# Kernel optimization log

Measured on AMD Instinct MI355X. Metric: run time of the kernel, lower is better.

Reference implementation:

```python
import jax, jax.numpy as jnp
import numpy as np

B, N, D = 64, 1024, 128
K = 6  # hardcoded neighbor count in the module


def setup_inputs() -> dict:
    key = jax.random.key(0)
    ks = jax.random.split(key, 11)
    def lin(k, out_d, in_d):
        kw, kb = jax.random.split(k)
        s = 1.0 / np.sqrt(in_d)
        W = jax.random.uniform(kw, (out_d, in_d), minval=-s, maxval=s, dtype=jnp.float32)
        b = jax.random.uniform(kb, (out_d,), minval=-s, maxval=s, dtype=jnp.float32)
        return W, b
    loc = jax.random.uniform(ks[0], (B, N, 2), dtype=jnp.float32)
    deadline = jax.random.uniform(ks[1], (B, N), dtype=jnp.float32)
    depot = jax.random.uniform(ks[2], (B, 2), dtype=jnp.float32)
    W3d, b3d = lin(ks[3], D, 3)
    W2d, b2d = lin(ks[4], D, 2)
    Wnb, bnb = lin(ks[5], D, K * D)
    Wdep, bdep = lin(ks[6], D, 2)
    return {"loc": loc, "deadline": deadline, "depot": depot,
            "W3d": W3d, "b3d": b3d, "W2d": W2d, "b2d": b2d,
            "Wnb": Wnb, "bnb": bnb, "Wdep": Wdep, "bdep": bdep}


def reference(loc, deadline, depot, W3d, b3d, W2d, b2d, Wnb, bnb, Wdep, bdep):
    x = jnp.concatenate([loc, deadline[:, :, None]], axis=2)  # [B,N,3]
    x2 = x[:, :, 0:2]                                          # [B,N,2]
    F2 = jnp.einsum('bnf,df->bnd', x2, W2d) + b2d              # [B,N,D]
    F3 = jnp.einsum('bnf,df->bnd', x, W3d) + b3d               # [B,N,D]
    # pairwise euclidean distances; indices are non-differentiable -> stop_gradient
    diff = x2[:, None, :, :] - x2[:, :, None, :]               # [B,N,N,2]
    dist = jnp.sqrt(jnp.sum(diff * diff, axis=-1))             # [B,N,N]
    _, neighbors = jax.lax.top_k(jax.lax.stop_gradient(-dist), K)  # [B,N,K] smallest dists (incl. self)
    # faithful quirk: original does F0_embedding_2d[:, neighbors][0] == gather from batch-0 embeddings
    nb = F2[0][neighbors]                                      # [B,N,K,D]
    nb_c = nb.reshape(nb.shape[0], nb.shape[1], K * nb.shape[3])  # [B,N,K*D]
    Fn = jnp.einsum('bnf,df->bnd', nb_c, Wnb) + bnb            # [B,N,D]
    Ff = Fn + F3
    dep = depot @ Wdep.T + bdep                                 # [B,D]
    h = jax.nn.leaky_relu(jnp.concatenate([dep[:, None, :], Ff], axis=1), negative_slope=0.01)
    return h, h.mean(axis=1)
```

## Files before the change

kernel.cpp:

```cpp
#include <hip/hip_runtime.h>
#include <hip/hip_bf16.h>

#define CB 64
#define CN 1024
#define CD 128
#define CK 6

typedef __attribute__((ext_vector_type(8))) short short8;
typedef __attribute__((ext_vector_type(4))) float floatx4;

__device__ __forceinline__ unsigned short f2bf(float f) {
    union { float f; unsigned u; } c; c.f = f;
    unsigned u = c.u;
    u += 0x7FFFu + ((u >> 16) & 1u);
    return (unsigned short)(u >> 16);
}

#define WS_G      0
#define WS_NBRS   3145728
#define WS_IDS    3932160
#define WS_STARTS 4063232
#define WS_PART   4129024

struct SortSM { float2 pts[CN]; int cnt[256]; int base[256]; };
struct GSM    { unsigned short As[128 * 40]; unsigned short Bs[128 * 40]; };
union GridSM  { SortSM s; GSM g; };

__global__ void __launch_bounds__(256) k_gridg(
    const float* __restrict__ loc,
    const float* __restrict__ W2d,
    const float* __restrict__ b2d,
    const float* __restrict__ Wnb,
    unsigned short* __restrict__ ids,
    int* __restrict__ starts,
    float* __restrict__ G)
{
    __shared__ GridSM sm;
    int t = threadIdx.x;

    if (blockIdx.x < 64) {
        int b = blockIdx.x;
        const float2* lb = (const float2*)loc + b * CN;
#pragma unroll
        for (int r = 0; r < 4; ++r) sm.s.pts[t + r * 256] = lb[t + r * 256];
        sm.s.cnt[t] = 0;
        __syncthreads();
        int mycell[4];
#pragma unroll
        for (int r = 0; r < 4; ++r) {
            float2 p = sm.s.pts[t * 4 + r];
            int cx = (int)(p.x * 16.0f); cx = cx > 15 ? 15 : cx;
            int cy = (int)(p.y * 16.0f); cy = cy > 15 ? 15 : cy;
            mycell[r] = (cy << 4) + cx;
            atomicAdd(&sm.s.cnt[mycell[r]], 1);
        }
        __syncthreads();
        for (int off = 1; off < 256; off <<= 1) {
            int u = (t >= off) ? sm.s.cnt[t - off] : 0;
            __syncthreads();
            sm.s.cnt[t] += u;
            __syncthreads();
        }
        int excl = (t == 0) ? 0 : sm.s.cnt[t - 1];
        sm.s.base[t] = excl;
        starts[b * 257 + t] = excl;
        if (t == 255) starts[b * 257 + 256] = sm.s.cnt[255];
        __syncthreads();
#pragma unroll
        for (int r = 0; r < 4; ++r) {
            int pos = atomicAdd(&sm.s.base[mycell[r]], 1);
            ids[b * CN + pos] = (unsigned short)(t * 4 + r);
        }
        return;
    }

    int gb = blockIdx.x - 64;
    int k = gb % 6;
    int tile = gb / 6;
    int n0 = tile << 7;

    int wave = t >> 6, lane = t & 63;
    int koff = (lane >> 4) * 8;
    int mrow = lane & 15;

    int e2 = t & 15, rg = t >> 4;
    float2 pl[8];
#pragma unroll
    for (int rr = 0; rr < 8; ++rr)
        pl[rr] = ((const float2*)loc)[n0 + rg + rr * 16];

    int bd = t >> 1, bhalf = t & 1;

    floatx4 acc[2][8];
#pragma unroll
    for (int i = 0; i < 2; ++i)
#pragma unroll
        for (int j = 0; j < 8; ++j) acc[i][j] = (floatx4){0.f, 0.f, 0.f, 0.f};

#pragma unroll
    for (int c = 0; c < 4; ++c) {
        __syncthreads();
        {
            int e0 = c * 32 + e2 * 2;
            float wx0 = W2d[e0 * 2],     wy0 = W2d[e0 * 2 + 1], bz0 = b2d[e0];
            float wx1 = W2d[e0 * 2 + 2], wy1 = W2d[e0 * 2 + 3], bz1 = b2d[e0 + 1];
#pragma unroll
            for (int rr = 0; rr < 8; ++rr) {
                float2 p = pl[rr];
                float v0 = fmaf(p.x, wx0, fmaf(p.y, wy0, bz0));
                float v1 = fmaf(p.x, wx1, fmaf(p.y, wy1, bz1));
                unsigned pack = (unsigned)f2bf(v0) | ((unsigned)f2bf(v1) << 16);
                *(unsigned*)&sm.g.As[(rg + rr * 16) * 40 + e2 * 2] = pack;
            }
        }
        {
            const float* src = Wnb + bd * 768 + k * 128 + c * 32 + bhalf * 16;
            float4 f0 = *(const float4*)(src);
            float4 f1 = *(const float4*)(src + 4);
            float4 f2v = *(const float4*)(src + 8);
            float4 f3 = *(const float4*)(src + 12);
            uint4 o0, o1;
            o0.x = (unsigned)f2bf(f0.x) | ((unsigned)f2bf(f0.y) << 16);
            o0.y = (unsigned)f2bf(f0.z) | ((unsigned)f2bf(f0.w) << 16);
            o0.z = (unsigned)f2bf(f1.x) | ((unsigned)f2bf(f1.y) << 16);
            o0.w = (unsigned)f2bf(f1.z) | ((unsigned)f2bf(f1.w) << 16);
            o1.x = (unsigned)f2bf(f2v.x) | ((unsigned)f2bf(f2v.y) << 16);
            o1.y = (unsigned)f2bf(f2v.z) | ((unsigned)f2bf(f2v.w) << 16);
            o1.z = (unsigned)f2bf(f3.x) | ((unsigned)f2bf(f3.y) << 16);
            o1.w = (unsigned)f2bf(f3.z) | ((unsigned)f2bf(f3.w) << 16);
            *(uint4*)&sm.g.Bs[bd * 40 + bhalf * 16] = o0;
            *(uint4*)&sm.g.Bs[bd * 40 + bhalf * 16 + 8] = o1;
        }
        __syncthreads();
        short8 af[2];
#pragma unroll
        for (int i = 0; i < 2; ++i)
            af[i] = *(const short8*)&sm.g.As[(wave * 32 + i * 16 + mrow) * 40 + koff];
#pragma unroll
        for (int j = 0; j < 8; ++j) {
            short8 bfr = *(const short8*)&sm.g.Bs[(j * 16 + mrow) * 40 + koff];
#pragma unroll
            for (int i = 0; i < 2; ++i)
                acc[i][j] = __builtin_amdgcn_mfma_f32_16x16x32_bf16(
                    af[i], bfr, acc[i][j], 0, 0, 0);
        }
    }

    int lq = lane >> 4, lc = lane & 15;
#pragma unroll
    for (int j = 0; j < 8; ++j) {
        int d = j * 16 + lc;
#pragma unroll
        for (int i = 0; i < 2; ++i) {
#pragma unroll
            for (int r = 0; r < 4; ++r) {
                int row = wave * 32 + i * 16 + lq * 4 + r;
                G[(n0 + row) * 768 + k * 128 + d] = acc[i][j][r];
            }
        }
    }
}

__global__ void __launch_bounds__(256) k_knn(
    const float* __restrict__ loc,
    const unsigned short* __restrict__ ids,
    const int* __restrict__ starts,
    unsigned short* __restrict__ nbrs)
{
    __shared__ float2 xy_tmp[CN];
    __shared__ float2 xy_s[CN];
    __shared__ unsigned short ids_s[CN];
    __shared__ int st_s[257];
    int t = threadIdx.x;
    int b = blockIdx.x >> 4;
    int qbase = (blockIdx.x & 15) << 6;
    const float2* lb = (const float2*)loc + b * CN;
#pragma unroll
    for (int r = 0; r < 4; ++r) {
        int p = t + r * 256;
        xy_tmp[p] = lb[p];
        ids_s[p] = ids[b * CN + p];
    }
    st_s[t] = starts[b * 257 + t];
    if (t == 0) st_s[256] = starts[b * 257 + 256];
    __syncthreads();
#pragma unroll
    for (int r = 0; r < 4; ++r) {
        int p = t + r * 256;
        xy_s[p] = xy_tmp[ids_s[p]];
    }
    __syncthreads();

    int qp = qbase + (t >> 2);
    int pi = t & 3;
    int q = ids_s[qp];
    float2 qxy = xy_s[qp];
    float xq = qxy.x, yq = qxy.y;
    int cx = (int)(xq * 16.0f); cx = cx > 15 ? 15 : cx;
    int cy = (int)(yq * 16.0f); cy = cy > 15 ? 15 : cy;
    float dk[CK]; int ik[CK];
#pragma unroll
    for (int s = 0; s < CK; ++s) { dk[s] = 1e30f; ik[s] = 0x7FFFFFFF; }
    float dk5sq = __builtin_inff();
    const float h = 0.0625f;

#define KNN_CAND(P)                                                        \
    {                                                                      \
        float2 v = xy_s[P];                                                \
        float dx = __fsub_rn(v.x, xq);                                     \
        float dy = __fsub_rn(v.y, yq);                                     \
        float d2 = __fadd_rn(__fmul_rn(dx, dx), __fmul_rn(dy, dy));        \
        if (d2 < dk5sq) {                                                  \
            float ds = __fsqrt_rn(d2);                                     \
            int j = ids_s[P];                                              \
            if (ds < dk[CK - 1] || (ds == dk[CK - 1] && j < ik[CK - 1])) { \
                float dc = ds; int jc = j;                                 \
                _Pragma("unroll")                                          \
                for (int s = 0; s < CK; ++s) {                             \
                    bool sw = (dc < dk[s]) || (dc == dk[s] && jc < ik[s]); \
                    float od = dk[s]; int oi = ik[s];                      \
                    dk[s] = sw ? dc : od; ik[s] = sw ? jc : oi;            \
                    dc = sw ? od : dc;    jc = sw ? oi : jc;               \
                }                                                          \
                if (ik[CK - 1] != 0x7FFFFFFF)                              \
                    dk5sq = __fmul_rn(dk[CK - 1], dk[CK - 1]) * 1.000001f; \
            }                                                              \
        }                                                                  \
    }

    {
        int yl = cy > 0 ? cy - 1 : 0, yh = cy < 15 ? cy + 1 : 15;
        int xl = cx > 0 ? cx - 1 : 0, xh = cx < 15 ? cx + 1 : 15;
        for (int yy = yl; yy <= yh; ++yy) {
            int p  = st_s[(yy << 4) + xl] + pi;
            int pe = st_s[(yy << 4) + xh + 1];
            for (; p < pe; p += 4) KNN_CAND(p)
        }
    }
    bool done;
    {
        int x0 = cx - 1, x1 = cx + 1, y0 = cy - 1, y1 = cy + 1;
        done = (x0 <= 0 && y0 <= 0 && x1 >= 15 && y1 >= 15);
        float mL = x0 > 0  ? __fsub_rn(xq, (float)x0 * h)       : 1e30f;
        float mR = x1 < 15 ? __fsub_rn((float)(x1 + 1) * h, xq) : 1e30f;
        float mB = y0 > 0  ? __fsub_rn(yq, (float)y0 * h)       : 1e30f;
        float mT = y1 < 15 ? __fsub_rn((float)(y1 + 1) * h, yq) : 1e30f;
        float bound = fminf(fminf(mL, mR), fminf(mB, mT)) * 0.999999f;
        done = done || (ik[CK - 1] != 0x7FFFFFFF && dk[CK - 1] < bound);
    }
    if (!done) {
        for (int r = 2; r < 16; ++r) {
            int x0 = cx - r, x1 = cx + r, y0 = cy - r, y1 = cy + r;
            int yl = y0 < 0 ? 0 : y0, yh = y1 > 15 ? 15 : y1;
            int xl = x0 < 0 ? 0 : x0, xh = x1 > 15 ? 15 : x1;
            for (int yy = yl; yy <= yh; ++yy) {
                bool ey = (yy == y0) || (yy == y1);
                if (ey) {
                    int p  = st_s[(yy << 4) + xl] + pi;
                    int pe = st_s[(yy << 4) + xh + 1];
                    for (; p < pe; p += 4) KNN_CAND(p)
                } else {
                    if (x0 >= 0) {
                        int p  = st_s[(yy << 4) + x0] + pi;
                        int pe = st_s[(yy << 4) + x0 + 1];
                        for (; p < pe; p += 4) KNN_CAND(p)
                    }
                    if (x1 <= 15) {
                        int p  = st_s[(yy << 4) + x1] + pi;
                        int pe = st_s[(yy << 4) + x1 + 1];
                        for (; p < pe; p += 4) KNN_CAND(p)
                    }
                }
            }
            if (x0 <= 0 && y0 <= 0 && x1 >= 15 && y1 >= 15) break;
            float mL = x0 > 0  ? __fsub_rn(xq, (float)x0 * h)       : 1e30f;
            float mR = x1 < 15 ? __fsub_rn((float)(x1 + 1) * h, xq) : 1e30f;
            float mB = y0 > 0  ? __fsub_rn(yq, (float)y0 * h)       : 1e30f;
            float mT = y1 < 15 ? __fsub_rn((float)(y1 + 1) * h, yq) : 1e30f;
            float bound = fminf(fminf(mL, mR), fminf(mB, mT)) * 0.999999f;
            if (ik[CK - 1] != 0x7FFFFFFF && dk[CK - 1] < bound) break;
        }
    }
#undef KNN_CAND

#define KNN_MERGE(MASK)                                                     \
    {                                                                       \
        float od[CK]; int oi[CK];                                           \
        _Pragma("unroll")                                                   \
        for (int s = 0; s < CK; ++s) {                                      \
            od[s] = __shfl_xor(dk[s], MASK);                                \
            oi[s] = __shfl_xor(ik[s], MASK);                                \
        }                                                                   \
        _Pragma("unroll")                                                   \
        for (int e = 0; e < CK; ++e) {                                      \
            float dc = od[e]; int jc = oi[e];                               \
            if ((dc < dk[CK - 1]) || (dc == dk[CK - 1] && jc < ik[CK - 1])) { \
                _Pragma("unroll")                                           \
                for (int s = 0; s < CK; ++s) {                              \
                    bool sw = (dc < dk[s]) || (dc == dk[s] && jc < ik[s]);  \
                    float td = dk[s]; int ti = ik[s];                       \
                    dk[s] = sw ? dc : td; ik[s] = sw ? jc : ti;             \
                    dc = sw ? td : dc;    jc = sw ? ti : jc;                \
                }                                                           \
            }                                                               \
        }                                                                   \
    }
    KNN_MERGE(1)
    KNN_MERGE(2)
#undef KNN_MERGE

    if (pi == 0) {
        unsigned short* o = nbrs + (unsigned)(b * CN + q) * CK;
#pragma unroll
        for (int s = 0; s < CK; ++s) o[s] = (unsigned short)ik[s];
    }
}

__global__ void __launch_bounds__(256) k_gather(
    const float* __restrict__ loc,
    const float* __restrict__ dl,
    const unsigned short* __restrict__ nbrs,
    const float* __restrict__ G,
    const float* __restrict__ W3d,
    const float* __restrict__ b3d,
    const float* __restrict__ bnb,
    float* __restrict__ outh,
    float* __restrict__ partials)
{
    __shared__ float psum[4][CD];
    __shared__ unsigned short nbs[64 * CK];
    int t = threadIdx.x, bx = blockIdx.x;
    int rowbase = bx << 6, b = rowbase >> 10;

    if (t < 192)
        ((unsigned*)nbs)[t] = ((const unsigned*)(nbrs + (size_t)rowbase * CK))[t];

    int d4 = t & 31, rg = t >> 5;
    int d0 = d4 * 4;
    float4 w0, w1, w2, bias;
#pragma unroll
    for (int dd = 0; dd < 4; ++dd) {
        int d = d0 + dd;
        ((float*)&w0)[dd] = W3d[d * 3];
        ((float*)&w1)[dd] = W3d[d * 3 + 1];
        ((float*)&w2)[dd] = W3d[d * 3 + 2];
        ((float*)&bias)[dd] = b3d[d] + bnb[d];
    }
    float4 csum = {0.f, 0.f, 0.f, 0.f};
    __syncthreads();

#pragma unroll
    for (int rr = 0; rr < 4; ++rr) {
        int r0 = rr * 16 + rg;
        int r1 = r0 + 8;
        int gr0 = rowbase + r0, gr1 = rowbase + r1;
        const unsigned short* nA = nbs + r0 * CK;
        const unsigned short* nB = nbs + r1 * CK;
        float4 ga0 = *(const float4*)(G + nA[0] * 768 + 0 * 128 + d0);
        float4 ga1 = *(const float4*)(G + nA[1] * 768 + 1 * 128 + d0);
        float4 ga2 = *(const float4*)(G + nA[2] * 768 + 2 * 128 + d0);
        float4 ga3 = *(const float4*)(G + nA[3] * 768 + 3 * 128 + d0);
        float4 ga4 = *(const float4*)(G + nA[4] * 768 + 4 * 128 + d0);
        float4 ga5 = *(const float4*)(G + nA[5] * 768 + 5 * 128 + d0);
        float4 gb0 = *(const float4*)(G + nB[0] * 768 + 0 * 128 + d0);
        float4 gb1 = *(const float4*)(G + nB[1] * 768 + 1 * 128 + d0);
        float4 gb2 = *(const float4*)(G + nB[2] * 768 + 2 * 128 + d0);
        float4 gb3 = *(const float4*)(G + nB[3] * 768 + 3 * 128 + d0);
        float4 gb4 = *(const float4*)(G + nB[4] * 768 + 4 * 128 + d0);
        float4 gb5 = *(const float4*)(G + nB[5] * 768 + 5 * 128 + d0);
        float2 lA = ((const float2*)loc)[gr0];
        float2 lB = ((const float2*)loc)[gr1];
        float dA = dl[gr0];
        float dB = dl[gr1];
        {
            float4 a;
            a.x = ((((ga0.x + ga1.x) + ga2.x) + ga3.x) + ga4.x) + ga5.x;
            a.y = ((((ga0.y + ga1.y) + ga2.y) + ga3.y) + ga4.y) + ga5.y;
            a.z = ((((ga0.z + ga1.z) + ga2.z) + ga3.z) + ga4.z) + ga5.z;
            a.w = ((((ga0.w + ga1.w) + ga2.w) + ga3.w) + ga4.w) + ga5.w;
            float4 v;
            v.x = a.x + bias.x + lA.x * w0.x + lA.y * w1.x + dA * w2.x;
            v.y = a.y + bias.y + lA.x * w0.y + lA.y * w1.y + dA * w2.y;
            v.z = a.z + bias.z + lA.x * w0.z + lA.y * w1.z + dA * w2.z;
            v.w = a.w + bias.w + lA.x * w0.w + lA.y * w1.w + dA * w2.w;
            float4 lr;
            lr.x = v.x >= 0.f ? v.x : 0.01f * v.x;
            lr.y = v.y >= 0.f ? v.y : 0.01f * v.y;
            lr.z = v.z >= 0.f ? v.z : 0.01f * v.z;
            lr.w = v.w >= 0.f ? v.w : 0.01f * v.w;
            *(float4*)(outh + ((long)b * 1025 + (gr0 & 1023) + 1) * 128 + d0) = lr;
            csum.x += lr.x; csum.y += lr.y; csum.z += lr.z; csum.w += lr.w;
        }
        {
            float4 a;
            a.x = ((((gb0.x + gb1.x) + gb2.x) + gb3.x) + gb4.x) + gb5.x;
            a.y = ((((gb0.y + gb1.y) + gb2.y) + gb3.y) + gb4.y) + gb5.y;
            a.z = ((((gb0.z + gb1.z) + gb2.z) + gb3.z) + gb4.z) + gb5.z;
            a.w = ((((gb0.w + gb1.w) + gb2.w) + gb3.w) + gb4.w) + gb5.w;
            float4 v;
            v.x = a.x + bias.x + lB.x * w0.x + lB.y * w1.x + dB * w2.x;
            v.y = a.y + bias.y + lB.x * w0.y + lB.y * w1.y + dB * w2.y;
            v.z = a.z + bias.z + lB.x * w0.z + lB.y * w1.z + dB * w2.z;
            v.w = a.w + bias.w + lB.x * w0.w + lB.y * w1.w + dB * w2.w;
            float4 lr;
            lr.x = v.x >= 0.f ? v.x : 0.01f * v.x;
            lr.y = v.y >= 0.f ? v.y : 0.01f * v.y;
            lr.z = v.z >= 0.f ? v.z : 0.01f * v.z;
            lr.w = v.w >= 0.f ? v.w : 0.01f * v.w;
            *(float4*)(outh + ((long)b * 1025 + (gr1 & 1023) + 1) * 128 + d0) = lr;
            csum.x += lr.x; csum.y += lr.y; csum.z += lr.z; csum.w += lr.w;
        }
    }

    csum.x += __shfl_xor(csum.x, 32);
    csum.y += __shfl_xor(csum.y, 32);
    csum.z += __shfl_xor(csum.z, 32);
    csum.w += __shfl_xor(csum.w, 32);
    int wave = t >> 6, lane = t & 63;
    if (lane < 32) {
        psum[wave][d0]     = csum.x;
        psum[wave][d0 + 1] = csum.y;
        psum[wave][d0 + 2] = csum.z;
        psum[wave][d0 + 3] = csum.w;
    }
    __syncthreads();
    if (t < CD)
        partials[(bx << 7) + t] =
            psum[0][t] + psum[1][t] + psum[2][t] + psum[3][t];
}

__global__ void k_fin(const float* __restrict__ depot,
                      const float* __restrict__ Wdep,
                      const float* __restrict__ bdep,
                      const float* __restrict__ partials,
                      float* __restrict__ out) {
    int idx = blockIdx.x * 256 + threadIdx.x;
    int b = idx >> 7, d = idx & 127;
    float acc = 0.f;
#pragma unroll
    for (int g = 0; g < 16; ++g) acc += partials[(b * 16 + g) * 128 + d];
    float dv = depot[b * 2] * Wdep[d * 2] + depot[b * 2 + 1] * Wdep[d * 2 + 1] + bdep[d];
    float lr = dv >= 0.f ? dv : 0.01f * dv;
    out[(long)b * 1025 * 128 + d] = lr;
    out[(long)CB * 1025 * 128 + idx] = (acc + lr) * (1.0f / 1025.0f);
}

extern "C" void kernel_launch(void* const* d_in, const int* in_sizes, int n_in,
                              void* d_out, int out_size, void* d_ws, size_t ws_size,
                              hipStream_t stream) {
    const float* loc      = (const float*)d_in[0];
    const float* deadline = (const float*)d_in[1];
    const float* depot    = (const float*)d_in[2];
    const float* W3d      = (const float*)d_in[3];
    const float* b3d      = (const float*)d_in[4];
    const float* W2d      = (const float*)d_in[5];
    const float* b2d      = (const float*)d_in[6];
    const float* Wnb      = (const float*)d_in[7];
    const float* bnb      = (const float*)d_in[8];
    const float* Wdep     = (const float*)d_in[9];
    const float* bdep     = (const float*)d_in[10];
    float* out = (float*)d_out;

    char* ws = (char*)d_ws;
    float* G              = (float*)(ws + WS_G);
    unsigned short* nbrs  = (unsigned short*)(ws + WS_NBRS);
    unsigned short* ids   = (unsigned short*)(ws + WS_IDS);
    int* starts           = (int*)(ws + WS_STARTS);
    float* partials       = (float*)(ws + WS_PART);

    k_gridg<<<112, 256, 0, stream>>>(loc, W2d, b2d, Wnb, ids, starts, G);
    k_knn<<<1024, 256, 0, stream>>>(loc, ids, starts, nbrs);
    k_gather<<<1024, 256, 0, stream>>>(loc, deadline, nbrs, G, W3d, b3d, bnb,
                                       out, partials);
    k_fin<<<32, 256, 0, stream>>>(depot, Wdep, bdep, partials, out);
}
```

Measured before the change: 134.5 us.

## Fuse final mean reduction into gather kernel via atomics and last-block finish

Removes the separate k_fin launch by having each gather block atomically add its column partial sums into a per-batch accumulator, with a counter-based last-block pattern writing the depot row and mean. Gather blocks are halved to 32 rows each (2048 blocks) with a launch bound of 6 blocks/CU to increase parallelism. Accumulators are zeroed in the first kernel. This trades a kernel launch for global atomics and nondeterministic float summation order.

```diff
diff --git a/kernel.cpp b/kernel.cpp
--- a/kernel.cpp
+++ b/kernel.cpp
@@ -20,7 +20,8 @@
 #define WS_NBRS   3145728
 #define WS_IDS    3932160
 #define WS_STARTS 4063232
-#define WS_PART   4129024
+#define WS_BSUM   4129024
+#define WS_CNT    4161792
 
 struct SortSM { float2 pts[CN]; int cnt[256]; int base[256]; };
 struct GSM    { unsigned short As[128 * 40]; unsigned short Bs[128 * 40]; };
@@ -33,13 +34,17 @@
     const float* __restrict__ Wnb,
     unsigned short* __restrict__ ids,
     int* __restrict__ starts,
-    float* __restrict__ G)
+    float* __restrict__ G,
+    float* __restrict__ bsum,
+    int* __restrict__ cnt)
 {
     __shared__ GridSM sm;
     int t = threadIdx.x;
 
     if (blockIdx.x < 64) {
         int b = blockIdx.x;
+        if (t < 128) bsum[(b << 7) + t] = 0.f;
+        if (t == 128) cnt[b] = 0;
         const float2* lb = (const float2*)loc + b * CN;
 #pragma unroll
         for (int r = 0; r < 4; ++r) sm.s.pts[t + r * 256] = lb[t + r * 256];
@@ -316,7 +321,7 @@
     }
 }
 
-__global__ void __launch_bounds__(256) k_gather(
+__global__ void __launch_bounds__(256, 6) k_gatherfin(
     const float* __restrict__ loc,
     const float* __restrict__ dl,
     const unsigned short* __restrict__ nbrs,
@@ -324,15 +329,20 @@
     const float* __restrict__ W3d,
     const float* __restrict__ b3d,
     const float* __restrict__ bnb,
-    float* __restrict__ outh,
-    float* __restrict__ partials)
+    const float* __restrict__ depot,
+    const float* __restrict__ Wdep,
+    const float* __restrict__ bdep,
+    float* __restrict__ out,
+    float* __restrict__ bsum,
+    int* __restrict__ cnt)
 {
     __shared__ float psum[4][CD];
-    __shared__ unsigned short nbs[64 * CK];
+    __shared__ unsigned short nbs[32 * CK];
+    __shared__ int lastflag;
     int t = threadIdx.x, bx = blockIdx.x;
-    int rowbase = bx << 6, b = rowbase >> 10;
-
-    if (t < 192)
+    int rowbase = bx << 5, b = bx >> 5;
+
+    if (t < 96)
         ((unsigned*)nbs)[t] = ((const unsigned*)(nbrs + (size_t)rowbase * CK))[t];
 
     int d4 = t & 31, rg = t >> 5;
@@ -350,7 +360,7 @@
     __syncthreads();
 
 #pragma unroll
-    for (int rr = 0; rr < 4; ++rr) {
+    for (int rr = 0; rr < 2; ++rr) {
         int r0 = rr * 16 + rg;
         int r1 = r0 + 8;
         int gr0 = rowbase + r0, gr1 = rowbase + r1;
@@ -388,7 +398,7 @@
             lr.y = v.y >= 0.f ? v.y : 0.01f * v.y;
             lr.z = v.z >= 0.f ? v.z : 0.01f * v.z;
             lr.w = v.w >= 0.f ? v.w : 0.01f * v.w;
-            *(float4*)(outh + ((long)b * 1025 + (gr0 & 1023) + 1) * 128 + d0) = lr;
+            *(float4*)(out + ((long)b * 1025 + (gr0 & 1023) + 1) * 128 + d0) = lr;
             csum.x += lr.x; csum.y += lr.y; csum.z += lr.z; csum.w += lr.w;
         }
         {
@@ -407,7 +417,7 @@
             lr.y = v.y >= 0.f ? v.y : 0.01f * v.y;
             lr.z = v.z >= 0.f ? v.z : 0.01f * v.z;
             lr.w = v.w >= 0.f ? v.w : 0.01f * v.w;
-            *(float4*)(outh + ((long)b * 1025 + (gr1 & 1023) + 1) * 128 + d0) = lr;
+            *(float4*)(out + ((long)b * 1025 + (gr1 & 1023) + 1) * 128 + d0) = lr;
             csum.x += lr.x; csum.y += lr.y; csum.z += lr.z; csum.w += lr.w;
         }
     }
@@ -425,24 +435,24 @@
     }
     __syncthreads();
     if (t < CD)
-        partials[(bx << 7) + t] =
-            psum[0][t] + psum[1][t] + psum[2][t] + psum[3][t];
-}
-
-__global__ void k_fin(const float* __restrict__ depot,
-                      const float* __restrict__ Wdep,
-                      const float* __restrict__ bdep,
-                      const float* __restrict__ partials,
-                      float* __restrict__ out) {
-    int idx = blockIdx.x * 256 + threadIdx.x;
-    int b = idx >> 7, d = idx & 127;
-    float acc = 0.f;
-#pragma unroll
-    for (int g = 0; g < 16; ++g) acc += partials[(b * 16 + g) * 128 + d];
-    float dv = depot[b * 2] * Wdep[d * 2] + depot[b * 2 + 1] * Wdep[d * 2 + 1] + bdep[d];
-    float lr = dv >= 0.f ? dv : 0.01f * dv;
-    out[(long)b * 1025 * 128 + d] = lr;
-    out[(long)CB * 1025 * 128 + idx] = (acc + lr) * (1.0f / 1025.0f);
+        atomicAdd(bsum + (b << 7) + t,
+                  psum[0][t] + psum[1][t] + psum[2][t] + psum[3][t]);
+    __syncthreads();
+    if (t == 0) {
+        __threadfence();
+        int old = atomicAdd(cnt + b, 1);
+        lastflag = (old == 31);
+    }
+    __syncthreads();
+    if (lastflag && t < CD) {
+        float acc = atomicAdd(bsum + (b << 7) + t, 0.0f);
+        float dv = depot[b * 2] * Wdep[t * 2] + depot[b * 2 + 1] * Wdep[t * 2 + 1]
+                 + bdep[t];
+        float lr = dv >= 0.f ? dv : 0.01f * dv;
+        out[(long)b * 1025 * 128 + t] = lr;
+        out[(long)CB * 1025 * 128 + (b << 7) + t] =
+            (acc + lr) * (1.0f / 1025.0f);
+    }
 }
 
 extern "C" void kernel_launch(void* const* d_in, const int* in_sizes, int n_in,
@@ -466,11 +476,13 @@
     unsigned short* nbrs  = (unsigned short*)(ws + WS_NBRS);
     unsigned short* ids   = (unsigned short*)(ws + WS_IDS);
     int* starts           = (int*)(ws + WS_STARTS);
-    float* partials       = (float*)(ws + WS_PART);
-
-    k_gridg<<<112, 256, 0, stream>>>(loc, W2d, b2d, Wnb, ids, starts, G);
+    float* bsum           = (float*)(ws + WS_BSUM);
+    int* cnt              = (int*)(ws + WS_CNT);
+
+    k_gridg<<<112, 256, 0, stream>>>(loc, W2d, b2d, Wnb, ids, starts, G,
+                                     bsum, cnt);
     k_knn<<<1024, 256, 0, stream>>>(loc, ids, starts, nbrs);
-    k_gather<<<1024, 256, 0, stream>>>(loc, deadline, nbrs, G, W3d, b3d, bnb,
-                                       out, partials);
-    k_fin<<<32, 256, 0, stream>>>(depot, Wdep, bdep, partials, out);
+    k_gatherfin<<<2048, 256, 0, stream>>>(loc, deadline, nbrs, G, W3d, b3d,
+                                          bnb, depot, Wdep, bdep, out,
+                                          bsum, cnt);
 }
```

Result: slower. 193.7 us (+44.1%).
